# Performance work log

Measured on AMD Instinct MI355X. Metric: run time of the kernel, lower is better.

The kernel has to match this reference:

```python
import jax, jax.numpy as jnp
import numpy as np

N_NODES = 50000
N_EDGES = 800000
IN_DIM, HIDDEN, Z_DIM = 32, 64, 32


def gcn_conv(x, W, b, src, dst, n):
    """PyG-style GCNConv: h = D^{-1/2}(A+I)D^{-1/2} (x W) + b."""
    h = x @ W  # [N, out]
    loop = jnp.arange(n, dtype=src.dtype)
    s = jnp.concatenate([src, loop])  # add self-loops
    d = jnp.concatenate([dst, loop])
    deg = jax.ops.segment_sum(jnp.ones(s.shape, h.dtype), d, num_segments=n)
    dinv = jax.lax.rsqrt(jnp.maximum(deg, jnp.asarray(1.0, h.dtype)))
    norm = dinv[s] * dinv[d]                       # [E+N]
    msg = h[s] * norm[:, None]                     # gather + scale
    out = jax.ops.segment_sum(msg, d, num_segments=n)  # scatter-add
    return out + b


def setup_inputs() -> dict:
    key = jax.random.key(0)
    ks = jax.random.split(key, 8)
    sc = lambda fan_in: 1.0 / np.sqrt(fan_in)
    x = jax.random.normal(ks[0], (N_NODES, IN_DIM), jnp.float32)
    edge_index = jax.random.randint(ks[1], (2, N_EDGES), 0, N_NODES, jnp.int64)
    W1 = jax.random.normal(ks[2], (IN_DIM, HIDDEN), jnp.float32) * sc(IN_DIM)
    b1 = jnp.zeros((HIDDEN,), jnp.float32)
    W2 = jax.random.normal(ks[3], (HIDDEN, HIDDEN), jnp.float32) * sc(HIDDEN)
    b2 = jnp.zeros((HIDDEN,), jnp.float32)
    W_mu = jax.random.normal(ks[4], (HIDDEN, Z_DIM), jnp.float32) * sc(HIDDEN)
    b_mu = jnp.zeros((Z_DIM,), jnp.float32)
    W_lv = jax.random.normal(ks[5], (HIDDEN, Z_DIM), jnp.float32) * sc(HIDDEN)
    b_lv = jnp.zeros((Z_DIM,), jnp.float32)
    eps = jax.random.normal(ks[6], (N_NODES, Z_DIM), jnp.float32)
    return {"x": x, "edge_index": edge_index, "W1": W1, "b1": b1, "W2": W2,
            "b2": b2, "W_mu": W_mu, "b_mu": b_mu, "W_lv": W_lv, "b_lv": b_lv,
            "eps": eps}


def reference(x, edge_index, W1, b1, W2, b2, W_mu, b_mu, W_lv, b_lv, eps):
    src, dst = edge_index[0], edge_index[1]
    n = x.shape[0]
    h = jax.nn.relu(gcn_conv(x, W1, b1, src, dst, n))
    h = jax.nn.relu(gcn_conv(h, W2, b2, src, dst, n))
    # dropout p=0.0 -> identity
    mu = gcn_conv(h, W_mu, b_mu, src, dst, n)
    logvar = gcn_conv(h, W_lv, b_lv, src, dst, n)
    z = mu + jnp.exp(0.5 * logvar) * eps  # reparametrize
    return (z, mu, logvar)
```

## Files before the change

kernel.cpp:

```cpp
#include <hip/hip_runtime.h>
#include <math.h>

#define N_NODES 50000
#define N_EDGES 800000
#define IN_DIM 32
#define HIDDEN 64
#define Z_DIM 32
#define SCAN_B 256
#define NB_SCAN ((N_NODES + SCAN_B - 1) / SCAN_B)
#define N_XCD 8
#define NPX ((N_NODES + N_XCD - 1) / N_XCD)
#define SLICE 2048
#define N_SLICE ((N_EDGES + SLICE - 1) / SLICE)
#define SCAT_B (N_SLICE * N_XCD)
#define FB 1024
#define CPAD 16

__device__ __forceinline__ unsigned short f2bf(float f) {
    unsigned int u = __float_as_uint(f);
    u += 0x7fffu + ((u >> 16) & 1u);
    return (unsigned short)(u >> 16);
}

__device__ __forceinline__ int detect64(const int* raw) {
    int lane = threadIdx.x & 63;
    int odd = raw[2 * lane + 1];
    unsigned long long b = __ballot(odd != 0);
    return (b == 0ULL) ? 1 : 0;
}

__device__ __forceinline__ void fma8(float w, uint4 f, float acc[8]) {
    acc[0] = fmaf(w, __uint_as_float(f.x << 16),         acc[0]);
    acc[1] = fmaf(w, __uint_as_float(f.x & 0xffff0000u), acc[1]);
    acc[2] = fmaf(w, __uint_as_float(f.y << 16),         acc[2]);
    acc[3] = fmaf(w, __uint_as_float(f.y & 0xffff0000u), acc[3]);
    acc[4] = fmaf(w, __uint_as_float(f.z << 16),         acc[4]);
    acc[5] = fmaf(w, __uint_as_float(f.z & 0xffff0000u), acc[5]);
    acc[6] = fmaf(w, __uint_as_float(f.w << 16),         acc[6]);
    acc[7] = fmaf(w, __uint_as_float(f.w & 0xffff0000u), acc[7]);
}
__device__ __forceinline__ void mul8(float w, uint4 f, float acc[8]) {
    acc[0] = w * __uint_as_float(f.x << 16);
    acc[1] = w * __uint_as_float(f.x & 0xffff0000u);
    acc[2] = w * __uint_as_float(f.y << 16);
    acc[3] = w * __uint_as_float(f.y & 0xffff0000u);
    acc[4] = w * __uint_as_float(f.z << 16);
    acc[5] = w * __uint_as_float(f.z & 0xffff0000u);
    acc[6] = w * __uint_as_float(f.w << 16);
    acc[7] = w * __uint_as_float(f.w & 0xffff0000u);
}

__global__ void prep_a_kernel(const float* __restrict__ x, unsigned short* __restrict__ xb,
                              const void* __restrict__ raw, ushort2* __restrict__ ep0,
                              int* __restrict__ cnt) {
    int is64 = detect64((const int*)raw);
    int i = blockIdx.x * 256 + threadIdx.x;
    if (i < N_NODES * IN_DIM) xb[i] = f2bf(x[i]);
    if (i < N_NODES * CPAD) cnt[i] = 0;
    if (i < N_EDGES) {
        int s, d;
        if (is64) {
            s = (int)((const long long*)raw)[i];
            d = (int)((const long long*)raw)[N_EDGES + i];
        } else {
            s = ((const int*)raw)[i];
            d = ((const int*)raw)[N_EDGES + i];
        }
        ep0[i] = make_ushort2((unsigned short)s, (unsigned short)d);
    }
}

__global__ __launch_bounds__(256) void hist_kernel(const ushort2* __restrict__ ep0,
                                                   int* __restrict__ cnt,
                                                   unsigned short* __restrict__ rank) {
    int xcd = blockIdx.x % N_XCD;
    int sl  = blockIdx.x / N_XCD;
    int lo  = xcd * NPX, hi = lo + NPX;
    int base = sl * SLICE;
#pragma unroll
    for (int j = 0; j < SLICE / 256; j++) {
        int e = base + j * 256 + threadIdx.x;
        if (e < N_EDGES) {
            int d = ep0[e].y;
            if (d >= lo && d < hi)
                rank[e] = (unsigned short)atomicAdd(&cnt[(size_t)d * CPAD], 1);
        }
    }
}

__global__ void scan1_kernel(const int* __restrict__ cnt, int* __restrict__ pre,
                             int* __restrict__ bsum, float* __restrict__ dinv) {
    __shared__ int s[SCAN_B];
    int t = threadIdx.x;
    int g = blockIdx.x * SCAN_B + t;
    int v = (g < N_NODES) ? cnt[(size_t)g * CPAD] : 0;
    if (g < N_NODES) dinv[g] = rsqrtf((float)(v + 1));
    s[t] = v;
    __syncthreads();
    for (int o = 1; o < SCAN_B; o <<= 1) {
        int add = (t >= o) ? s[t - o] : 0;
        __syncthreads();
        s[t] += add;
        __syncthreads();
    }
    if (g < N_NODES) pre[g] = s[t] - v;
    if (t == SCAN_B - 1) bsum[blockIdx.x] = s[t];
}

#define BSUM_SCAN_PROLOGUE(bsum, sb, sx)                                    \
    {                                                                       \
        int t_ = threadIdx.x;                                               \
        int bv_ = (t_ < NB_SCAN) ? bsum[t_] : 0;                            \
        sb[t_] = bv_;                                                       \
        __syncthreads();                                                    \
        for (int o_ = 1; o_ < 256; o_ <<= 1) {                              \
            int a_ = (t_ >= o_) ? sb[t_ - o_] : 0;                          \
            __syncthreads();                                                \
            sb[t_] += a_;                                                   \
            __syncthreads();                                                \
        }                                                                   \
        sx[t_] = sb[t_] - bv_;                                              \
        __syncthreads();                                                    \
    }

__global__ __launch_bounds__(256) void scatter_kernel(
        const ushort2* __restrict__ ep0, const unsigned short* __restrict__ rank,
        const int* __restrict__ pre, const int* __restrict__ bsum,
        const float* __restrict__ dinv, int2* __restrict__ ep) {
    __shared__ int sb[256];
    __shared__ int sx[256];
    BSUM_SCAN_PROLOGUE(bsum, sb, sx)
    int base = blockIdx.x * SLICE;
#pragma unroll
    for (int j = 0; j < SLICE / 256; j++) {
        int e = base + j * 256 + threadIdx.x;
        if (e < N_EDGES) {
            ushort2 sd = ep0[e];
            int d = sd.y;
            int p = pre[d] + sx[d >> 8] + (int)rank[e];
            int s = sd.x;
            ep[p] = make_int2(s, __float_as_int(dinv[s]));
        }
    }
}

__device__ __forceinline__ void agg64(int e0, int e1, int2 pr,
                                      const int2* __restrict__ ep,
                                      const uint4* __restrict__ g4,
                                      int2* eb, int lane, int gsel, int c,
                                      float acc[8]) {
    for (int b0 = e0; b0 < e1; b0 += 64) {
        int cnt = e1 - b0; cnt = cnt > 64 ? 64 : cnt;
        eb[lane] = pr;
        for (int j = 0; j < cnt; j += 16) {
            int2 ew0 = eb[j + gsel];
            int2 ew1 = eb[j + 8 + gsel];
            uint4 f0 = g4[(size_t)ew0.x * 8 + c];
            uint4 f1 = g4[(size_t)ew1.x * 8 + c];
            fma8(__int_as_float(ew0.y), f0, acc);
            fma8(__int_as_float(ew1.y), f1, acc);
        }
        if (b0 + 64 < e1) {
            pr = make_int2(0, 0);
            int idx = b0 + 64 + lane;
            if (idx < e1) pr = ep[idx];
        }
    }
}

__device__ __forceinline__ void agg32(int e0, int e1, int2 pr,
                                      const int2* __restrict__ ep,
                                      const uint4* __restrict__ x4,
                                      int2* eb, int lane, int gsel, int c,
                                      float acc[8]) {
    for (int b0 = e0; b0 < e1; b0 += 64) {
        int cnt = e1 - b0; cnt = cnt > 64 ? 64 : cnt;
        eb[lane] = pr;
        for (int j = 0; j < cnt; j += 32) {
            int2 ew0 = eb[j + gsel];
            int2 ew1 = eb[j + 16 + gsel];
            uint4 f0 = x4[(size_t)ew0.x * 4 + c];
            uint4 f1 = x4[(size_t)ew1.x * 4 + c];
            fma8(__int_as_float(ew0.y), f0, acc);
            fma8(__int_as_float(ew1.y), f1, acc);
        }
        if (b0 + 64 < e1) {
            pr = make_int2(0, 0);
            int idx = b0 + 64 + lane;
            if (idx < e1) pr = ep[idx];
        }
    }
}

__global__ __launch_bounds__(256) void fused_layer32_kernel(
        const int* __restrict__ pre, const int* __restrict__ bsum,
        const int2* __restrict__ ep, const float* __restrict__ dinv,
        const unsigned short* __restrict__ xb,
        const float* __restrict__ W1, const float* __restrict__ b1,
        unsigned short* __restrict__ out) {
    __shared__ int sb[256];
    __shared__ int sx[256];
    __shared__ int2 ebuf[4][64];
    __shared__ float sq[4][32];
    BSUM_SCAN_PROLOGUE(bsum, sb, sx)
    int lane = threadIdx.x & 63;
    int wav  = threadIdx.x >> 6;
    int gsel = lane >> 2;
    int c    = lane & 3;
    const uint4* x4 = (const uint4*)xb;
    int2* eb = &ebuf[wav][0];
    float wcol[IN_DIM];
#pragma unroll
    for (int k = 0; k < IN_DIM; k++) wcol[k] = W1[k * 64 + lane];
    float bb = b1[lane];
    int wid = __builtin_amdgcn_readfirstlane((int)((blockIdx.x * blockDim.x + threadIdx.x) >> 6));
    int nw  = (gridDim.x * blockDim.x) >> 6;
    int v = wid;
    if (v >= N_NODES) return;
    int e0 = pre[v] + sx[v >> 8];
    int e1 = (v + 1 < N_NODES) ? pre[v + 1] + sx[(v + 1) >> 8] : N_EDGES;
    float dv = dinv[v];
    uint4 hv = x4[(size_t)v * 4 + c];
    int2 pr = make_int2(0, 0);
    if (lane < e1 - e0) pr = ep[e0 + lane];
    while (v < N_NODES) {
        int vn = v + nw;
        int e0n = 0, e1n = 0;
        float dvn = 0.0f;
        uint4 hvn = make_uint4(0, 0, 0, 0);
        int2 prn = make_int2(0, 0);
        if (vn < N_NODES) {
            e0n = pre[vn] + sx[vn >> 8];
            e1n = (vn + 1 < N_NODES) ? pre[vn + 1] + sx[(vn + 1) >> 8] : N_EDGES;
            dvn = dinv[vn];
            hvn = x4[(size_t)vn * 4 + c];
            if (lane < e1n - e0n) prn = ep[e0n + lane];
        }
        float sv = (gsel == 0) ? dv : 0.0f;
        float acc[8];
        mul8(sv, hv, acc);
        agg32(e0, e1, pr, ep, x4, eb, lane, gsel, c, acc);
#pragma unroll
        for (int i = 0; i < 8; i++) {
            acc[i] += __shfl_xor(acc[i], 4);
            acc[i] += __shfl_xor(acc[i], 8);
            acc[i] += __shfl_xor(acc[i], 16);
            acc[i] += __shfl_xor(acc[i], 32);
        }
        if (lane < 4) {
            float4* qd = (float4*)(&sq[wav][lane * 8]);
            qd[0] = make_float4(dv * acc[0], dv * acc[1], dv * acc[2], dv * acc[3]);
            qd[1] = make_float4(dv * acc[4], dv * acc[5], dv * acc[6], dv * acc[7]);
        }
        float o0 = bb, o1 = 0.0f, o2 = 0.0f, o3 = 0.0f;
        const float4* q4 = (const float4*)(&sq[wav][0]);
#pragma unroll
        for (int k = 0; k < IN_DIM / 4; k++) {
            float4 tq = q4[k];
            o0 = fmaf(tq.x, wcol[4 * k + 0], o0);
            o1 = fmaf(tq.y, wcol[4 * k + 1], o1);
            o2 = fmaf(tq.z, wcol[4 * k + 2], o2);
            o3 = fmaf(tq.w, wcol[4 * k + 3], o3);
        }
        float o = (o0 + o1) + (o2 + o3);
        out[(size_t)v * 64 + lane] = f2bf(fmaxf(o, 0.0f));
        v = vn; e0 = e0n; e1 = e1n; dv = dvn; hv = hvn; pr = prn;
    }
}

__global__ __launch_bounds__(256) void fused_layer64_kernel(
        const int* __restrict__ pre, const int* __restrict__ bsum,
        const int2* __restrict__ ep, const float* __restrict__ dinv,
        const unsigned short* __restrict__ g,
        const float* __restrict__ W, const float* __restrict__ bias,
        unsigned short* __restrict__ out) {
    __shared__ int sb[256];
    __shared__ int sx[256];
    __shared__ int2 ebuf[4][64];
    __shared__ float sq[4][64];
    BSUM_SCAN_PROLOGUE(bsum, sb, sx)
    int lane = threadIdx.x & 63;
    int wav  = threadIdx.x >> 6;
    int gsel = lane >> 3;
    int c    = lane & 7;
    const uint4* g4 = (const uint4*)g;
    int2* eb = &ebuf[wav][0];
    float wcol[HIDDEN];
#pragma unroll
    for (int k = 0; k < HIDDEN; k++) wcol[k] = W[k * 64 + lane];
    float bb = bias[lane];
    int wid = __builtin_amdgcn_readfirstlane((int)((blockIdx.x * blockDim.x + threadIdx.x) >> 6));
    int nw  = (gridDim.x * blockDim.x) >> 6;
    int v = wid;
    if (v >= N_NODES) return;
    int e0 = pre[v] + sx[v >> 8];
    int e1 = (v + 1 < N_NODES) ? pre[v + 1] + sx[(v + 1) >> 8] : N_EDGES;
    float dv = dinv[v];
    uint4 hv = g4[(size_t)v * 8 + c];
    int2 pr = make_int2(0, 0);
    if (lane < e1 - e0) pr = ep[e0 + lane];
    while (v < N_NODES) {
        int vn = v + nw;
        int e0n = 0, e1n = 0;
        float dvn = 0.0f;
        uint4 hvn = make_uint4(0, 0, 0, 0);
        int2 prn = make_int2(0, 0);
        if (vn < N_NODES) {
            e0n = pre[vn] + sx[vn >> 8];
            e1n = (vn + 1 < N_NODES) ? pre[vn + 1] + sx[(vn + 1) >> 8] : N_EDGES;
            dvn = dinv[vn];
            hvn = g4[(size_t)vn * 8 + c];
            if (lane < e1n - e0n) prn = ep[e0n + lane];
        }
        float sv = (gsel == 0) ? dv : 0.0f;
        float acc[8];
        mul8(sv, hv, acc);
        agg64(e0, e1, pr, ep, g4, eb, lane, gsel, c, acc);
#pragma unroll
        for (int i = 0; i < 8; i++) {
            acc[i] += __shfl_xor(acc[i], 8);
            acc[i] += __shfl_xor(acc[i], 16);
            acc[i] += __shfl_xor(acc[i], 32);
        }
        if (lane < 8) {
            float4* qd = (float4*)(&sq[wav][lane * 8]);
            qd[0] = make_float4(dv * acc[0], dv * acc[1], dv * acc[2], dv * acc[3]);
            qd[1] = make_float4(dv * acc[4], dv * acc[5], dv * acc[6], dv * acc[7]);
        }
        float o0 = bb, o1 = 0.0f, o2 = 0.0f, o3 = 0.0f;
        const float4* q4 = (const float4*)(&sq[wav][0]);
#pragma unroll
        for (int k = 0; k < HIDDEN / 4; k++) {
            float4 tq = q4[k];
            o0 = fmaf(tq.x, wcol[4 * k + 0], o0);
            o1 = fmaf(tq.y, wcol[4 * k + 1], o1);
            o2 = fmaf(tq.z, wcol[4 * k + 2], o2);
            o3 = fmaf(tq.w, wcol[4 * k + 3], o3);
        }
        float o = (o0 + o1) + (o2 + o3);
        out[(size_t)v * 64 + lane] = f2bf(fmaxf(o, 0.0f));
        v = vn; e0 = e0n; e1 = e1n; dv = dvn; hv = hvn; pr = prn;
    }
}

__global__ __launch_bounds__(256) void fused_head_kernel(
        const int* __restrict__ pre, const int* __restrict__ bsum,
        const int2* __restrict__ ep, const float* __restrict__ dinv,
        const unsigned short* __restrict__ g,
        const float* __restrict__ Wmu, const float* __restrict__ Wlv,
        const float* __restrict__ bmu, const float* __restrict__ blv,
        const float* __restrict__ eps, float* __restrict__ outz) {
    __shared__ int sb[256];
    __shared__ int sx[256];
    __shared__ int2 ebuf[4][64];
    __shared__ float sq[4][64];
    BSUM_SCAN_PROLOGUE(bsum, sb, sx)
    int lane = threadIdx.x & 63;
    int wav  = threadIdx.x >> 6;
    int gsel = lane >> 3;
    int c    = lane & 7;
    int f = lane & 31;
    bool hi = lane >= 32;
    const uint4* g4 = (const uint4*)g;
    int2* eb = &ebuf[wav][0];
    float wcol[HIDDEN];
#pragma unroll
    for (int k = 0; k < HIDDEN; k++)
        wcol[k] = hi ? Wlv[k * 32 + f] : Wmu[k * 32 + f];
    float bb = hi ? blv[f] : bmu[f];
    float* z  = outz;
    float* mu = outz + (size_t)N_NODES * Z_DIM;
    float* lv = outz + 2 * (size_t)N_NODES * Z_DIM;
    int wid = __builtin_amdgcn_readfirstlane((int)((blockIdx.x * blockDim.x + threadIdx.x) >> 6));
    int nw  = (gridDim.x * blockDim.x) >> 6;
    int v = wid;
    if (v >= N_NODES) return;
    int e0 = pre[v] + sx[v >> 8];
    int e1 = (v + 1 < N_NODES) ? pre[v + 1] + sx[(v + 1) >> 8] : N_EDGES;
    float dv = dinv[v];
    uint4 hv = g4[(size_t)v * 8 + c];
    int2 pr = make_int2(0, 0);
    if (lane < e1 - e0) pr = ep[e0 + lane];
    while (v < N_NODES) {
        int vn = v + nw;
        int e0n = 0, e1n = 0;
        float dvn = 0.0f;
        uint4 hvn = make_uint4(0, 0, 0, 0);
        int2 prn = make_int2(0, 0);
        if (vn < N_NODES) {
            e0n = pre[vn] + sx[vn >> 8];
            e1n = (vn + 1 < N_NODES) ? pre[vn + 1] + sx[(vn + 1) >> 8] : N_EDGES;
            dvn = dinv[vn];
            hvn = g4[(size_t)vn * 8 + c];
            if (lane < e1n - e0n) prn = ep[e0n + lane];
        }
        float sv = (gsel == 0) ? dv : 0.0f;
        float acc[8];
        mul8(sv, hv, acc);
        agg64(e0, e1, pr, ep, g4, eb, lane, gsel, c, acc);
#pragma unroll
        for (int i = 0; i < 8; i++) {
            acc[i] += __shfl_xor(acc[i], 8);
            acc[i] += __shfl_xor(acc[i], 16);
            acc[i] += __shfl_xor(acc[i], 32);
        }
        if (lane < 8) {
            float4* qd = (float4*)(&sq[wav][lane * 8]);
            qd[0] = make_float4(dv * acc[0], dv * acc[1], dv * acc[2], dv * acc[3]);
            qd[1] = make_float4(dv * acc[4], dv * acc[5], dv * acc[6], dv * acc[7]);
        }
        float m0 = bb, m1 = 0.0f, m2 = 0.0f, m3 = 0.0f;
        const float4* q4 = (const float4*)(&sq[wav][0]);
#pragma unroll
        for (int k = 0; k < HIDDEN / 4; k++) {
            float4 tq = q4[k];
            m0 = fmaf(tq.x, wcol[4 * k + 0], m0);
            m1 = fmaf(tq.y, wcol[4 * k + 1], m1);
            m2 = fmaf(tq.z, wcol[4 * k + 2], m2);
            m3 = fmaf(tq.w, wcol[4 * k + 3], m3);
        }
        float m = (m0 + m1) + (m2 + m3);
        float ev = eps[(size_t)v * Z_DIM + f];
        float t  = expf(0.5f * m) * ev;
        float tlo = __shfl(t, lane | 32);
        size_t o = (size_t)v * Z_DIM + f;
        if (!hi) { mu[o] = m; z[o] = m + tlo; }
        else     { lv[o] = m; }
        v = vn; e0 = e0n; e1 = e1n; dv = dvn; hv = hvn; pr = prn;
    }
}

extern "C" void kernel_launch(void* const* d_in, const int* in_sizes, int n_in,
                              void* d_out, int out_size, void* d_ws, size_t ws_size,
                              hipStream_t stream) {
    const float* x   = (const float*)d_in[0];
    const void*  ei  = d_in[1];
    const float* W1  = (const float*)d_in[2];
    const float* b1  = (const float*)d_in[3];
    const float* W2  = (const float*)d_in[4];
    const float* b2  = (const float*)d_in[5];
    const float* Wmu = (const float*)d_in[6];
    const float* bmu = (const float*)d_in[7];
    const float* Wlv = (const float*)d_in[8];
    const float* blv = (const float*)d_in[9];
    const float* eps = (const float*)d_in[10];
    float* out = (float*)d_out;
    (void)in_sizes; (void)n_in; (void)out_size; (void)ws_size;

    char* ws = (char*)d_ws;
    size_t off = 0;
    auto alloc = [&](size_t bytes) -> void* {
        void* p = ws + off;
        off += (bytes + 255) & ~(size_t)255;
        return p;
    };
    int2*           ep     = (int2*)alloc(sizeof(int2) * N_EDGES);
    ushort2*        ep0    = (ushort2*)alloc(sizeof(ushort2) * N_EDGES);
    unsigned short* rank   = (unsigned short*)alloc(sizeof(short) * N_EDGES);
    int*            pre    = (int*)alloc(sizeof(int) * (N_NODES + 1));
    int*            cnt    = (int*)alloc(sizeof(int) * (size_t)N_NODES * CPAD);
    float*          dinv   = (float*)alloc(sizeof(float) * N_NODES);
    int*            bsum   = (int*)alloc(sizeof(int) * 256);
    unsigned short* xb     = (unsigned short*)alloc(sizeof(short) * (size_t)N_NODES * IN_DIM);
    unsigned short* G      = (unsigned short*)alloc(sizeof(short) * (size_t)N_NODES * HIDDEN);
    unsigned short* H      = (unsigned short*)alloc(sizeof(short) * (size_t)N_NODES * HIDDEN);

    prep_a_kernel<<<(N_NODES * IN_DIM + 255) / 256, 256, 0, stream>>>(x, xb, ei, ep0, cnt);
    hist_kernel<<<SCAT_B, 256, 0, stream>>>(ep0, cnt, rank);
    scan1_kernel<<<NB_SCAN, SCAN_B, 0, stream>>>(cnt, pre, bsum, dinv);
    scatter_kernel<<<N_SLICE, 256, 0, stream>>>(ep0, rank, pre, bsum, dinv, ep);
    fused_layer32_kernel<<<FB, 256, 0, stream>>>(pre, bsum, ep, dinv, xb, W1, b1, H);
    fused_layer64_kernel<<<FB, 256, 0, stream>>>(pre, bsum, ep, dinv, H, W2, b2, G);
    fused_head_kernel<<<FB, 256, 0, stream>>>(pre, bsum, ep, dinv, G, Wmu, Wlv, bmu, blv, eps, out);
}
```

Measured before the change: 249.1 us.

## Merge all seven kernels into one cooperative persistent kernel with grid syncs

Replaces the seven separate launches (prep, histogram, scan, scatter and three fused GCN layers) with a single cooperative kernel that runs each phase as a grid-stride loop and separates phases with grid-wide barriers. The aim is to remove per-launch overhead and the inter-kernel drain gaps. In exchange the grid shrinks to 512 blocks with a 2-blocks-per-SM launch bound, so there is less parallelism and fewer waves for latency hiding. The aggregation phases also keep a 64-entry weight column in registers across all phases, which raises register pressure.

```diff
diff --git a/kernel.cpp b/kernel.cpp
--- a/kernel.cpp
+++ b/kernel.cpp
@@ -1,5 +1,8 @@
 #include <hip/hip_runtime.h>
+#include <hip/hip_cooperative_groups.h>
 #include <math.h>
+
+namespace cg = cooperative_groups;
 
 #define N_NODES 50000
 #define N_EDGES 800000
@@ -12,9 +15,8 @@
 #define NPX ((N_NODES + N_XCD - 1) / N_XCD)
 #define SLICE 2048
 #define N_SLICE ((N_EDGES + SLICE - 1) / SLICE)
-#define SCAT_B (N_SLICE * N_XCD)
-#define FB 1024
 #define CPAD 16
+#define GRID 512
 
 __device__ __forceinline__ unsigned short f2bf(float f) {
     unsigned int u = __float_as_uint(f);
@@ -48,100 +50,6 @@
     acc[5] = w * __uint_as_float(f.z & 0xffff0000u);
     acc[6] = w * __uint_as_float(f.w << 16);
     acc[7] = w * __uint_as_float(f.w & 0xffff0000u);
-}
-
-__global__ void prep_a_kernel(const float* __restrict__ x, unsigned short* __restrict__ xb,
-                              const void* __restrict__ raw, ushort2* __restrict__ ep0,
-                              int* __restrict__ cnt) {
-    int is64 = detect64((const int*)raw);
-    int i = blockIdx.x * 256 + threadIdx.x;
-    if (i < N_NODES * IN_DIM) xb[i] = f2bf(x[i]);
-    if (i < N_NODES * CPAD) cnt[i] = 0;
-    if (i < N_EDGES) {
-        int s, d;
-        if (is64) {
-            s = (int)((const long long*)raw)[i];
-            d = (int)((const long long*)raw)[N_EDGES + i];
-        } else {
-            s = ((const int*)raw)[i];
-            d = ((const int*)raw)[N_EDGES + i];
-        }
-        ep0[i] = make_ushort2((unsigned short)s, (unsigned short)d);
-    }
-}
-
-__global__ __launch_bounds__(256) void hist_kernel(const ushort2* __restrict__ ep0,
-                                                   int* __restrict__ cnt,
-                                                   unsigned short* __restrict__ rank) {
-    int xcd = blockIdx.x % N_XCD;
-    int sl  = blockIdx.x / N_XCD;
-    int lo  = xcd * NPX, hi = lo + NPX;
-    int base = sl * SLICE;
-#pragma unroll
-    for (int j = 0; j < SLICE / 256; j++) {
-        int e = base + j * 256 + threadIdx.x;
-        if (e < N_EDGES) {
-            int d = ep0[e].y;
-            if (d >= lo && d < hi)
-                rank[e] = (unsigned short)atomicAdd(&cnt[(size_t)d * CPAD], 1);
-        }
-    }
-}
-
-__global__ void scan1_kernel(const int* __restrict__ cnt, int* __restrict__ pre,
-                             int* __restrict__ bsum, float* __restrict__ dinv) {
-    __shared__ int s[SCAN_B];
-    int t = threadIdx.x;
-    int g = blockIdx.x * SCAN_B + t;
-    int v = (g < N_NODES) ? cnt[(size_t)g * CPAD] : 0;
-    if (g < N_NODES) dinv[g] = rsqrtf((float)(v + 1));
-    s[t] = v;
-    __syncthreads();
-    for (int o = 1; o < SCAN_B; o <<= 1) {
-        int add = (t >= o) ? s[t - o] : 0;
-        __syncthreads();
-        s[t] += add;
-        __syncthreads();
-    }
-    if (g < N_NODES) pre[g] = s[t] - v;
-    if (t == SCAN_B - 1) bsum[blockIdx.x] = s[t];
-}
-
-#define BSUM_SCAN_PROLOGUE(bsum, sb, sx)                                    \
-    {                                                                       \
-        int t_ = threadIdx.x;                                               \
-        int bv_ = (t_ < NB_SCAN) ? bsum[t_] : 0;                            \
-        sb[t_] = bv_;                                                       \
-        __syncthreads();                                                    \
-        for (int o_ = 1; o_ < 256; o_ <<= 1) {                              \
-            int a_ = (t_ >= o_) ? sb[t_ - o_] : 0;                          \
-            __syncthreads();                                                \
-            sb[t_] += a_;                                                   \
-            __syncthreads();                                                \
-        }                                                                   \
-        sx[t_] = sb[t_] - bv_;                                              \
-        __syncthreads();                                                    \
-    }
-
-__global__ __launch_bounds__(256) void scatter_kernel(
-        const ushort2* __restrict__ ep0, const unsigned short* __restrict__ rank,
-        const int* __restrict__ pre, const int* __restrict__ bsum,
-        const float* __restrict__ dinv, int2* __restrict__ ep) {
-    __shared__ int sb[256];
-    __shared__ int sx[256];
-    BSUM_SCAN_PROLOGUE(bsum, sb, sx)
-    int base = blockIdx.x * SLICE;
-#pragma unroll
-    for (int j = 0; j < SLICE / 256; j++) {
-        int e = base + j * 256 + threadIdx.x;
-        if (e < N_EDGES) {
-            ushort2 sd = ep0[e];
-            int d = sd.y;
-            int p = pre[d] + sx[d >> 8] + (int)rank[e];
-            int s = sd.x;
-            ep[p] = make_int2(s, __float_as_int(dinv[s]));
-        }
-    }
 }
 
 __device__ __forceinline__ void agg64(int e0, int e1, int2 pr,
@@ -192,241 +100,311 @@
     }
 }
 
-__global__ __launch_bounds__(256) void fused_layer32_kernel(
-        const int* __restrict__ pre, const int* __restrict__ bsum,
-        const int2* __restrict__ ep, const float* __restrict__ dinv,
-        const unsigned short* __restrict__ xb,
+__global__ __launch_bounds__(256, 2) void mega_kernel(
+        const float* __restrict__ x, const void* __restrict__ raw,
         const float* __restrict__ W1, const float* __restrict__ b1,
-        unsigned short* __restrict__ out) {
-    __shared__ int sb[256];
-    __shared__ int sx[256];
-    __shared__ int2 ebuf[4][64];
-    __shared__ float sq[4][32];
-    BSUM_SCAN_PROLOGUE(bsum, sb, sx)
-    int lane = threadIdx.x & 63;
-    int wav  = threadIdx.x >> 6;
-    int gsel = lane >> 2;
-    int c    = lane & 3;
-    const uint4* x4 = (const uint4*)xb;
+        const float* __restrict__ W2, const float* __restrict__ b2,
+        const float* __restrict__ Wmu, const float* __restrict__ bmu,
+        const float* __restrict__ Wlv, const float* __restrict__ blv,
+        const float* __restrict__ eps, float* __restrict__ outz,
+        int2* __restrict__ ep, ushort2* __restrict__ ep0,
+        unsigned short* __restrict__ rank, int* __restrict__ pre,
+        int* __restrict__ cnt, float* __restrict__ dinv,
+        int* __restrict__ bsum, unsigned short* __restrict__ xb,
+        unsigned short* __restrict__ G, unsigned short* __restrict__ H) {
+    cg::grid_group gg = cg::this_grid();
+    __shared__ int   sb[256];
+    __shared__ int   sx[256];
+    __shared__ int2  ebuf[4][64];
+    __shared__ float sq[4][64];
+
+    const int tid  = threadIdx.x;
+    const int nthr = GRID * 256;
+    const int gi0  = (int)blockIdx.x * 256 + tid;
+    const int lane = tid & 63;
+    const int wav  = tid >> 6;
     int2* eb = &ebuf[wav][0];
-    float wcol[IN_DIM];
-#pragma unroll
-    for (int k = 0; k < IN_DIM; k++) wcol[k] = W1[k * 64 + lane];
-    float bb = b1[lane];
-    int wid = __builtin_amdgcn_readfirstlane((int)((blockIdx.x * blockDim.x + threadIdx.x) >> 6));
-    int nw  = (gridDim.x * blockDim.x) >> 6;
-    int v = wid;
-    if (v >= N_NODES) return;
-    int e0 = pre[v] + sx[v >> 8];
-    int e1 = (v + 1 < N_NODES) ? pre[v + 1] + sx[(v + 1) >> 8] : N_EDGES;
-    float dv = dinv[v];
-    uint4 hv = x4[(size_t)v * 4 + c];
-    int2 pr = make_int2(0, 0);
-    if (lane < e1 - e0) pr = ep[e0 + lane];
-    while (v < N_NODES) {
-        int vn = v + nw;
-        int e0n = 0, e1n = 0;
-        float dvn = 0.0f;
-        uint4 hvn = make_uint4(0, 0, 0, 0);
-        int2 prn = make_int2(0, 0);
-        if (vn < N_NODES) {
-            e0n = pre[vn] + sx[vn >> 8];
-            e1n = (vn + 1 < N_NODES) ? pre[vn + 1] + sx[(vn + 1) >> 8] : N_EDGES;
-            dvn = dinv[vn];
-            hvn = x4[(size_t)vn * 4 + c];
-            if (lane < e1n - e0n) prn = ep[e0n + lane];
-        }
-        float sv = (gsel == 0) ? dv : 0.0f;
-        float acc[8];
-        mul8(sv, hv, acc);
-        agg32(e0, e1, pr, ep, x4, eb, lane, gsel, c, acc);
-#pragma unroll
-        for (int i = 0; i < 8; i++) {
-            acc[i] += __shfl_xor(acc[i], 4);
-            acc[i] += __shfl_xor(acc[i], 8);
-            acc[i] += __shfl_xor(acc[i], 16);
-            acc[i] += __shfl_xor(acc[i], 32);
-        }
-        if (lane < 4) {
-            float4* qd = (float4*)(&sq[wav][lane * 8]);
-            qd[0] = make_float4(dv * acc[0], dv * acc[1], dv * acc[2], dv * acc[3]);
-            qd[1] = make_float4(dv * acc[4], dv * acc[5], dv * acc[6], dv * acc[7]);
-        }
-        float o0 = bb, o1 = 0.0f, o2 = 0.0f, o3 = 0.0f;
-        const float4* q4 = (const float4*)(&sq[wav][0]);
-#pragma unroll
-        for (int k = 0; k < IN_DIM / 4; k++) {
-            float4 tq = q4[k];
-            o0 = fmaf(tq.x, wcol[4 * k + 0], o0);
-            o1 = fmaf(tq.y, wcol[4 * k + 1], o1);
-            o2 = fmaf(tq.z, wcol[4 * k + 2], o2);
-            o3 = fmaf(tq.w, wcol[4 * k + 3], o3);
-        }
-        float o = (o0 + o1) + (o2 + o3);
-        out[(size_t)v * 64 + lane] = f2bf(fmaxf(o, 0.0f));
-        v = vn; e0 = e0n; e1 = e1n; dv = dvn; hv = hvn; pr = prn;
-    }
-}
-
-__global__ __launch_bounds__(256) void fused_layer64_kernel(
-        const int* __restrict__ pre, const int* __restrict__ bsum,
-        const int2* __restrict__ ep, const float* __restrict__ dinv,
-        const unsigned short* __restrict__ g,
-        const float* __restrict__ W, const float* __restrict__ bias,
-        unsigned short* __restrict__ out) {
-    __shared__ int sb[256];
-    __shared__ int sx[256];
-    __shared__ int2 ebuf[4][64];
-    __shared__ float sq[4][64];
-    BSUM_SCAN_PROLOGUE(bsum, sb, sx)
-    int lane = threadIdx.x & 63;
-    int wav  = threadIdx.x >> 6;
-    int gsel = lane >> 3;
-    int c    = lane & 7;
-    const uint4* g4 = (const uint4*)g;
-    int2* eb = &ebuf[wav][0];
+
+    int is64 = detect64((const int*)raw);
+    for (int i = gi0; i < N_NODES * IN_DIM; i += nthr) xb[i] = f2bf(x[i]);
+    for (int i = gi0; i < N_NODES * CPAD; i += nthr) cnt[i] = 0;
+    if (is64) {
+        const long long* r = (const long long*)raw;
+        for (int e = gi0; e < N_EDGES; e += nthr)
+            ep0[e] = make_ushort2((unsigned short)(int)r[e],
+                                  (unsigned short)(int)r[N_EDGES + e]);
+    } else {
+        const int* r = (const int*)raw;
+        for (int e = gi0; e < N_EDGES; e += nthr)
+            ep0[e] = make_ushort2((unsigned short)r[e],
+                                  (unsigned short)r[N_EDGES + e]);
+    }
+    gg.sync();
+
+    {
+        int xcd = (int)blockIdx.x & (N_XCD - 1);
+        int lo = xcd * NPX, hi2 = lo + NPX;
+        int nslb = GRID / N_XCD;
+        for (int sl = (int)blockIdx.x >> 3; sl < N_SLICE; sl += nslb) {
+            int base = sl * SLICE;
+#pragma unroll
+            for (int j = 0; j < SLICE / 256; j++) {
+                int e = base + j * 256 + tid;
+                if (e < N_EDGES) {
+                    int d = ep0[e].y;
+                    if (d >= lo && d < hi2)
+                        rank[e] = (unsigned short)atomicAdd(&cnt[(size_t)d * CPAD], 1);
+                }
+            }
+        }
+    }
+    gg.sync();
+
+    if (blockIdx.x < NB_SCAN) {
+        int g = (int)blockIdx.x * SCAN_B + tid;
+        int vv = (g < N_NODES) ? cnt[(size_t)g * CPAD] : 0;
+        if (g < N_NODES) dinv[g] = rsqrtf((float)(vv + 1));
+        sb[tid] = vv;
+        __syncthreads();
+        for (int o = 1; o < SCAN_B; o <<= 1) {
+            int add = (tid >= o) ? sb[tid - o] : 0;
+            __syncthreads();
+            sb[tid] += add;
+            __syncthreads();
+        }
+        if (g < N_NODES) pre[g] = sb[tid] - vv;
+        if (tid == SCAN_B - 1) bsum[blockIdx.x] = sb[tid];
+    }
+    gg.sync();
+
+    {
+        int bv = (tid < NB_SCAN) ? bsum[tid] : 0;
+        sb[tid] = bv;
+        __syncthreads();
+        for (int o = 1; o < 256; o <<= 1) {
+            int a = (tid >= o) ? sb[tid - o] : 0;
+            __syncthreads();
+            sb[tid] += a;
+            __syncthreads();
+        }
+        sx[tid] = sb[tid] - bv;
+        __syncthreads();
+    }
+
+    for (int e = gi0; e < N_EDGES; e += nthr) {
+        ushort2 sd = ep0[e];
+        int d = sd.y;
+        int p = pre[d] + sx[d >> 8] + (int)rank[e];
+        int s = sd.x;
+        ep[p] = make_int2(s, __float_as_int(dinv[s]));
+    }
+    gg.sync();
+
+    const int wid = __builtin_amdgcn_readfirstlane(gi0 >> 6);
+    const int nw  = nthr >> 6;
     float wcol[HIDDEN];
-#pragma unroll
-    for (int k = 0; k < HIDDEN; k++) wcol[k] = W[k * 64 + lane];
-    float bb = bias[lane];
-    int wid = __builtin_amdgcn_readfirstlane((int)((blockIdx.x * blockDim.x + threadIdx.x) >> 6));
-    int nw  = (gridDim.x * blockDim.x) >> 6;
-    int v = wid;
-    if (v >= N_NODES) return;
-    int e0 = pre[v] + sx[v >> 8];
-    int e1 = (v + 1 < N_NODES) ? pre[v + 1] + sx[(v + 1) >> 8] : N_EDGES;
-    float dv = dinv[v];
-    uint4 hv = g4[(size_t)v * 8 + c];
-    int2 pr = make_int2(0, 0);
-    if (lane < e1 - e0) pr = ep[e0 + lane];
-    while (v < N_NODES) {
-        int vn = v + nw;
-        int e0n = 0, e1n = 0;
-        float dvn = 0.0f;
-        uint4 hvn = make_uint4(0, 0, 0, 0);
-        int2 prn = make_int2(0, 0);
-        if (vn < N_NODES) {
-            e0n = pre[vn] + sx[vn >> 8];
-            e1n = (vn + 1 < N_NODES) ? pre[vn + 1] + sx[(vn + 1) >> 8] : N_EDGES;
-            dvn = dinv[vn];
-            hvn = g4[(size_t)vn * 8 + c];
-            if (lane < e1n - e0n) prn = ep[e0n + lane];
-        }
-        float sv = (gsel == 0) ? dv : 0.0f;
-        float acc[8];
-        mul8(sv, hv, acc);
-        agg64(e0, e1, pr, ep, g4, eb, lane, gsel, c, acc);
-#pragma unroll
-        for (int i = 0; i < 8; i++) {
-            acc[i] += __shfl_xor(acc[i], 8);
-            acc[i] += __shfl_xor(acc[i], 16);
-            acc[i] += __shfl_xor(acc[i], 32);
-        }
-        if (lane < 8) {
-            float4* qd = (float4*)(&sq[wav][lane * 8]);
-            qd[0] = make_float4(dv * acc[0], dv * acc[1], dv * acc[2], dv * acc[3]);
-            qd[1] = make_float4(dv * acc[4], dv * acc[5], dv * acc[6], dv * acc[7]);
-        }
-        float o0 = bb, o1 = 0.0f, o2 = 0.0f, o3 = 0.0f;
-        const float4* q4 = (const float4*)(&sq[wav][0]);
-#pragma unroll
-        for (int k = 0; k < HIDDEN / 4; k++) {
-            float4 tq = q4[k];
-            o0 = fmaf(tq.x, wcol[4 * k + 0], o0);
-            o1 = fmaf(tq.y, wcol[4 * k + 1], o1);
-            o2 = fmaf(tq.z, wcol[4 * k + 2], o2);
-            o3 = fmaf(tq.w, wcol[4 * k + 3], o3);
-        }
-        float o = (o0 + o1) + (o2 + o3);
-        out[(size_t)v * 64 + lane] = f2bf(fmaxf(o, 0.0f));
-        v = vn; e0 = e0n; e1 = e1n; dv = dvn; hv = hvn; pr = prn;
-    }
-}
-
-__global__ __launch_bounds__(256) void fused_head_kernel(
-        const int* __restrict__ pre, const int* __restrict__ bsum,
-        const int2* __restrict__ ep, const float* __restrict__ dinv,
-        const unsigned short* __restrict__ g,
-        const float* __restrict__ Wmu, const float* __restrict__ Wlv,
-        const float* __restrict__ bmu, const float* __restrict__ blv,
-        const float* __restrict__ eps, float* __restrict__ outz) {
-    __shared__ int sb[256];
-    __shared__ int sx[256];
-    __shared__ int2 ebuf[4][64];
-    __shared__ float sq[4][64];
-    BSUM_SCAN_PROLOGUE(bsum, sb, sx)
-    int lane = threadIdx.x & 63;
-    int wav  = threadIdx.x >> 6;
-    int gsel = lane >> 3;
-    int c    = lane & 7;
-    int f = lane & 31;
-    bool hi = lane >= 32;
-    const uint4* g4 = (const uint4*)g;
-    int2* eb = &ebuf[wav][0];
-    float wcol[HIDDEN];
-#pragma unroll
-    for (int k = 0; k < HIDDEN; k++)
-        wcol[k] = hi ? Wlv[k * 32 + f] : Wmu[k * 32 + f];
-    float bb = hi ? blv[f] : bmu[f];
-    float* z  = outz;
-    float* mu = outz + (size_t)N_NODES * Z_DIM;
-    float* lv = outz + 2 * (size_t)N_NODES * Z_DIM;
-    int wid = __builtin_amdgcn_readfirstlane((int)((blockIdx.x * blockDim.x + threadIdx.x) >> 6));
-    int nw  = (gridDim.x * blockDim.x) >> 6;
-    int v = wid;
-    if (v >= N_NODES) return;
-    int e0 = pre[v] + sx[v >> 8];
-    int e1 = (v + 1 < N_NODES) ? pre[v + 1] + sx[(v + 1) >> 8] : N_EDGES;
-    float dv = dinv[v];
-    uint4 hv = g4[(size_t)v * 8 + c];
-    int2 pr = make_int2(0, 0);
-    if (lane < e1 - e0) pr = ep[e0 + lane];
-    while (v < N_NODES) {
-        int vn = v + nw;
-        int e0n = 0, e1n = 0;
-        float dvn = 0.0f;
-        uint4 hvn = make_uint4(0, 0, 0, 0);
-        int2 prn = make_int2(0, 0);
-        if (vn < N_NODES) {
-            e0n = pre[vn] + sx[vn >> 8];
-            e1n = (vn + 1 < N_NODES) ? pre[vn + 1] + sx[(vn + 1) >> 8] : N_EDGES;
-            dvn = dinv[vn];
-            hvn = g4[(size_t)vn * 8 + c];
-            if (lane < e1n - e0n) prn = ep[e0n + lane];
-        }
-        float sv = (gsel == 0) ? dv : 0.0f;
-        float acc[8];
-        mul8(sv, hv, acc);
-        agg64(e0, e1, pr, ep, g4, eb, lane, gsel, c, acc);
-#pragma unroll
-        for (int i = 0; i < 8; i++) {
-            acc[i] += __shfl_xor(acc[i], 8);
-            acc[i] += __shfl_xor(acc[i], 16);
-            acc[i] += __shfl_xor(acc[i], 32);
-        }
-        if (lane < 8) {
-            float4* qd = (float4*)(&sq[wav][lane * 8]);
-            qd[0] = make_float4(dv * acc[0], dv * acc[1], dv * acc[2], dv * acc[3]);
-            qd[1] = make_float4(dv * acc[4], dv * acc[5], dv * acc[6], dv * acc[7]);
-        }
-        float m0 = bb, m1 = 0.0f, m2 = 0.0f, m3 = 0.0f;
-        const float4* q4 = (const float4*)(&sq[wav][0]);
-#pragma unroll
-        for (int k = 0; k < HIDDEN / 4; k++) {
-            float4 tq = q4[k];
-            m0 = fmaf(tq.x, wcol[4 * k + 0], m0);
-            m1 = fmaf(tq.y, wcol[4 * k + 1], m1);
-            m2 = fmaf(tq.z, wcol[4 * k + 2], m2);
-            m3 = fmaf(tq.w, wcol[4 * k + 3], m3);
-        }
-        float m = (m0 + m1) + (m2 + m3);
-        float ev = eps[(size_t)v * Z_DIM + f];
-        float t  = expf(0.5f * m) * ev;
-        float tlo = __shfl(t, lane | 32);
-        size_t o = (size_t)v * Z_DIM + f;
-        if (!hi) { mu[o] = m; z[o] = m + tlo; }
-        else     { lv[o] = m; }
-        v = vn; e0 = e0n; e1 = e1n; dv = dvn; hv = hvn; pr = prn;
+
+    {
+        int gsel = lane >> 2;
+        int c    = lane & 3;
+        const uint4* x4 = (const uint4*)xb;
+#pragma unroll
+        for (int k = 0; k < IN_DIM; k++) wcol[k] = W1[k * 64 + lane];
+        float bb = b1[lane];
+        int v = wid;
+        int e0 = 0, e1 = 0;
+        float dv = 0.0f;
+        uint4 hv = make_uint4(0, 0, 0, 0);
+        int2 pr = make_int2(0, 0);
+        if (v < N_NODES) {
+            e0 = pre[v] + sx[v >> 8];
+            e1 = (v + 1 < N_NODES) ? pre[v + 1] + sx[(v + 1) >> 8] : N_EDGES;
+            dv = dinv[v];
+            hv = x4[(size_t)v * 4 + c];
+            if (lane < e1 - e0) pr = ep[e0 + lane];
+        }
+        while (v < N_NODES) {
+            int vn = v + nw;
+            int e0n = 0, e1n = 0;
+            float dvn = 0.0f;
+            uint4 hvn = make_uint4(0, 0, 0, 0);
+            int2 prn = make_int2(0, 0);
+            if (vn < N_NODES) {
+                e0n = pre[vn] + sx[vn >> 8];
+                e1n = (vn + 1 < N_NODES) ? pre[vn + 1] + sx[(vn + 1) >> 8] : N_EDGES;
+                dvn = dinv[vn];
+                hvn = x4[(size_t)vn * 4 + c];
+                if (lane < e1n - e0n) prn = ep[e0n + lane];
+            }
+            float sv = (gsel == 0) ? dv : 0.0f;
+            float acc[8];
+            mul8(sv, hv, acc);
+            agg32(e0, e1, pr, ep, x4, eb, lane, gsel, c, acc);
+#pragma unroll
+            for (int i = 0; i < 8; i++) {
+                acc[i] += __shfl_xor(acc[i], 4);
+                acc[i] += __shfl_xor(acc[i], 8);
+                acc[i] += __shfl_xor(acc[i], 16);
+                acc[i] += __shfl_xor(acc[i], 32);
+            }
+            if (lane < 4) {
+                float4* qd = (float4*)(&sq[wav][lane * 8]);
+                qd[0] = make_float4(dv * acc[0], dv * acc[1], dv * acc[2], dv * acc[3]);
+                qd[1] = make_float4(dv * acc[4], dv * acc[5], dv * acc[6], dv * acc[7]);
+            }
+            float o0 = bb, o1 = 0.0f, o2 = 0.0f, o3 = 0.0f;
+            const float4* q4 = (const float4*)(&sq[wav][0]);
+#pragma unroll
+            for (int k = 0; k < IN_DIM / 4; k++) {
+                float4 tq = q4[k];
+                o0 = fmaf(tq.x, wcol[4 * k + 0], o0);
+                o1 = fmaf(tq.y, wcol[4 * k + 1], o1);
+                o2 = fmaf(tq.z, wcol[4 * k + 2], o2);
+                o3 = fmaf(tq.w, wcol[4 * k + 3], o3);
+            }
+            float o = (o0 + o1) + (o2 + o3);
+            H[(size_t)v * 64 + lane] = f2bf(fmaxf(o, 0.0f));
+            v = vn; e0 = e0n; e1 = e1n; dv = dvn; hv = hvn; pr = prn;
+        }
+    }
+    gg.sync();
+
+    {
+        int gsel = lane >> 3;
+        int c    = lane & 7;
+        const uint4* g4 = (const uint4*)H;
+#pragma unroll
+        for (int k = 0; k < HIDDEN; k++) wcol[k] = W2[k * 64 + lane];
+        float bb = b2[lane];
+        int v = wid;
+        int e0 = 0, e1 = 0;
+        float dv = 0.0f;
+        uint4 hv = make_uint4(0, 0, 0, 0);
+        int2 pr = make_int2(0, 0);
+        if (v < N_NODES) {
+            e0 = pre[v] + sx[v >> 8];
+            e1 = (v + 1 < N_NODES) ? pre[v + 1] + sx[(v + 1) >> 8] : N_EDGES;
+            dv = dinv[v];
+            hv = g4[(size_t)v * 8 + c];
+            if (lane < e1 - e0) pr = ep[e0 + lane];
+        }
+        while (v < N_NODES) {
+            int vn = v + nw;
+            int e0n = 0, e1n = 0;
+            float dvn = 0.0f;
+            uint4 hvn = make_uint4(0, 0, 0, 0);
+            int2 prn = make_int2(0, 0);
+            if (vn < N_NODES) {
+                e0n = pre[vn] + sx[vn >> 8];
+                e1n = (vn + 1 < N_NODES) ? pre[vn + 1] + sx[(vn + 1) >> 8] : N_EDGES;
+                dvn = dinv[vn];
+                hvn = g4[(size_t)vn * 8 + c];
+                if (lane < e1n - e0n) prn = ep[e0n + lane];
+            }
+            float sv = (gsel == 0) ? dv : 0.0f;
+            float acc[8];
+            mul8(sv, hv, acc);
+            agg64(e0, e1, pr, ep, g4, eb, lane, gsel, c, acc);
+#pragma unroll
+            for (int i = 0; i < 8; i++) {
+                acc[i] += __shfl_xor(acc[i], 8);
+                acc[i] += __shfl_xor(acc[i], 16);
+                acc[i] += __shfl_xor(acc[i], 32);
+            }
+            if (lane < 8) {
+                float4* qd = (float4*)(&sq[wav][lane * 8]);
+                qd[0] = make_float4(dv * acc[0], dv * acc[1], dv * acc[2], dv * acc[3]);
+                qd[1] = make_float4(dv * acc[4], dv * acc[5], dv * acc[6], dv * acc[7]);
+            }
+            float o0 = bb, o1 = 0.0f, o2 = 0.0f, o3 = 0.0f;
+            const float4* q4 = (const float4*)(&sq[wav][0]);
+#pragma unroll
+            for (int k = 0; k < HIDDEN / 4; k++) {
+                float4 tq = q4[k];
+                o0 = fmaf(tq.x, wcol[4 * k + 0], o0);
+                o1 = fmaf(tq.y, wcol[4 * k + 1], o1);
+                o2 = fmaf(tq.z, wcol[4 * k + 2], o2);
+                o3 = fmaf(tq.w, wcol[4 * k + 3], o3);
+            }
+            float o = (o0 + o1) + (o2 + o3);
+            G[(size_t)v * 64 + lane] = f2bf(fmaxf(o, 0.0f));
+            v = vn; e0 = e0n; e1 = e1n; dv = dvn; hv = hvn; pr = prn;
+        }
+    }
+    gg.sync();
+
+    {
+        int gsel = lane >> 3;
+        int c    = lane & 7;
+        int f    = lane & 31;
+        bool hi  = lane >= 32;
+        const uint4* g4 = (const uint4*)G;
+#pragma unroll
+        for (int k = 0; k < HIDDEN; k++)
+            wcol[k] = hi ? Wlv[k * 32 + f] : Wmu[k * 32 + f];
+        float bb = hi ? blv[f] : bmu[f];
+        float* z  = outz;
+        float* mu = outz + (size_t)N_NODES * Z_DIM;
+        float* lv = outz + 2 * (size_t)N_NODES * Z_DIM;
+        int v = wid;
+        int e0 = 0, e1 = 0;
+        float dv = 0.0f;
+        uint4 hv = make_uint4(0, 0, 0, 0);
+        int2 pr = make_int2(0, 0);
+        if (v < N_NODES) {
+            e0 = pre[v] + sx[v >> 8];
+            e1 = (v + 1 < N_NODES) ? pre[v + 1] + sx[(v + 1) >> 8] : N_EDGES;
+            dv = dinv[v];
+            hv = g4[(size_t)v * 8 + c];
+            if (lane < e1 - e0) pr = ep[e0 + lane];
+        }
+        while (v < N_NODES) {
+            int vn = v + nw;
+            int e0n = 0, e1n = 0;
+            float dvn = 0.0f;
+            uint4 hvn = make_uint4(0, 0, 0, 0);
+            int2 prn = make_int2(0, 0);
+            if (vn < N_NODES) {
+                e0n = pre[vn] + sx[vn >> 8];
+                e1n = (vn + 1 < N_NODES) ? pre[vn + 1] + sx[(vn + 1) >> 8] : N_EDGES;
+                dvn = dinv[vn];
+                hvn = g4[(size_t)vn * 8 + c];
+                if (lane < e1n - e0n) prn = ep[e0n + lane];
+            }
+            float sv = (gsel == 0) ? dv : 0.0f;
+            float acc[8];
+            mul8(sv, hv, acc);
+            agg64(e0, e1, pr, ep, g4, eb, lane, gsel, c, acc);
+#pragma unroll
+            for (int i = 0; i < 8; i++) {
+                acc[i] += __shfl_xor(acc[i], 8);
+                acc[i] += __shfl_xor(acc[i], 16);
+                acc[i] += __shfl_xor(acc[i], 32);
+            }
+            if (lane < 8) {
+                float4* qd = (float4*)(&sq[wav][lane * 8]);
+                qd[0] = make_float4(dv * acc[0], dv * acc[1], dv * acc[2], dv * acc[3]);
+                qd[1] = make_float4(dv * acc[4], dv * acc[5], dv * acc[6], dv * acc[7]);
+            }
+            float m0 = bb, m1 = 0.0f, m2 = 0.0f, m3 = 0.0f;
+            const float4* q4 = (const float4*)(&sq[wav][0]);
+#pragma unroll
+            for (int k = 0; k < HIDDEN / 4; k++) {
+                float4 tq = q4[k];
+                m0 = fmaf(tq.x, wcol[4 * k + 0], m0);
+                m1 = fmaf(tq.y, wcol[4 * k + 1], m1);
+                m2 = fmaf(tq.z, wcol[4 * k + 2], m2);
+                m3 = fmaf(tq.w, wcol[4 * k + 3], m3);
+            }
+            float m = (m0 + m1) + (m2 + m3);
+            float ev = eps[(size_t)v * Z_DIM + f];
+            float t  = expf(0.5f * m) * ev;
+            float tlo = __shfl(t, lane | 32);
+            size_t o = (size_t)v * Z_DIM + f;
+            if (!hi) { mu[o] = m; z[o] = m + tlo; }
+            else     { lv[o] = m; }
+            v = vn; e0 = e0n; e1 = e1n; dv = dvn; hv = hvn; pr = prn;
+        }
     }
 }
 
@@ -465,11 +443,15 @@
     unsigned short* G      = (unsigned short*)alloc(sizeof(short) * (size_t)N_NODES * HIDDEN);
     unsigned short* H      = (unsigned short*)alloc(sizeof(short) * (size_t)N_NODES * HIDDEN);
 
-    prep_a_kernel<<<(N_NODES * IN_DIM + 255) / 256, 256, 0, stream>>>(x, xb, ei, ep0, cnt);
-    hist_kernel<<<SCAT_B, 256, 0, stream>>>(ep0, cnt, rank);
-    scan1_kernel<<<NB_SCAN, SCAN_B, 0, stream>>>(cnt, pre, bsum, dinv);
-    scatter_kernel<<<N_SLICE, 256, 0, stream>>>(ep0, rank, pre, bsum, dinv, ep);
-    fused_layer32_kernel<<<FB, 256, 0, stream>>>(pre, bsum, ep, dinv, xb, W1, b1, H);
-    fused_layer64_kernel<<<FB, 256, 0, stream>>>(pre, bsum, ep, dinv, H, W2, b2, G);
-    fused_head_kernel<<<FB, 256, 0, stream>>>(pre, bsum, ep, dinv, G, Wmu, Wlv, bmu, blv, eps, out);
-}
+    void* kargs[] = {
+        (void*)&x, (void*)&ei,
+        (void*)&W1, (void*)&b1, (void*)&W2, (void*)&b2,
+        (void*)&Wmu, (void*)&bmu, (void*)&Wlv, (void*)&blv,
+        (void*)&eps, (void*)&out,
+        (void*)&ep, (void*)&ep0, (void*)&rank, (void*)&pre,
+        (void*)&cnt, (void*)&dinv, (void*)&bsum, (void*)&xb,
+        (void*)&G, (void*)&H
+    };
+    hipLaunchCooperativeKernel((void*)mega_kernel, dim3(GRID), dim3(256),
+                               kargs, 0, stream);
+}
```

Result: slower. 662.0 us (+165.8%).
